# Optimization experiments

Measured on AMD Instinct MI355X. Metric: run time of the kernel, lower is better.

Reference implementation:

```python
import jax, jax.numpy as jnp
import numpy as np

B, S, D, H = 8, 1024, 1024, 16
DH = D // H
EPS = 1e-5


def _layernorm(x):
    # elementwise_affine=False LayerNorm, eps=1e-5
    m = jnp.mean(x, axis=-1, keepdims=True)
    v = jnp.var(x, axis=-1, keepdims=True)
    return (x - m) * jax.lax.rsqrt(v + EPS)


def setup_inputs() -> dict:
    key = jax.random.key(0)
    ks = jax.random.split(key, 11)
    s = 0.02
    return {
        "x": jax.random.normal(ks[0], (B, S, D), jnp.float32),
        "y": jax.random.normal(ks[1], (B, 1, D), jnp.float32),
        "w_adaln": jax.random.normal(ks[2], (6 * D, D), jnp.float32) * s,
        "b_adaln": jnp.zeros((6 * D,), jnp.float32),
        "w_qkv": jax.random.normal(ks[3], (3 * D, D), jnp.float32) * s,
        "w_proj": jax.random.normal(ks[4], (D, D), jnp.float32) * s,
        "b_proj": jnp.zeros((D,), jnp.float32),
        "w_fc1": jax.random.normal(ks[5], (4 * D, D), jnp.float32) * s,
        "b_fc1": jnp.zeros((4 * D,), jnp.float32),
        "w_fc2": jax.random.normal(ks[6], (D, 4 * D), jnp.float32) * s,
        "b_fc2": jnp.zeros((D,), jnp.float32),
    }


def reference(x, y, w_adaln, b_adaln, w_qkv, w_proj, b_proj, w_fc1, b_fc1, w_fc2, b_fc2):
    # adaLN-Zero modulation params from conditioning y: SiLU -> Linear -> 6 chunks
    mods = jax.nn.silu(y) @ w_adaln.T + b_adaln          # [B,1,6D]
    sh_a, sc_a, g_a, sh_m, sc_m, g_m = jnp.split(mods, 6, axis=-1)

    # --- attention branch ---
    xm = _layernorm(x) * (1.0 + sc_a) + sh_a             # modulate
    qkv = xm @ w_qkv.T                                   # [B,S,3D] (qkv_bias=False)
    q, k, v = [t.reshape(B, S, H, DH).transpose(0, 2, 1, 3) for t in jnp.split(qkv, 3, axis=-1)]
    scale = 1.0 / np.sqrt(DH)
    scores = jnp.einsum("bhqd,bhkd->bhqk", q, k) * scale  # unfused MATH-backend sdpa
    attn = jax.nn.softmax(scores, axis=-1)
    o = jnp.einsum("bhqk,bhkd->bhqd", attn, v)
    o = o.transpose(0, 2, 1, 3).reshape(B, S, D)
    o = o @ w_proj.T + b_proj
    x = x + g_a * o                                      # gated residual

    # --- MLP branch ---
    xm = _layernorm(x) * (1.0 + sc_m) + sh_m
    h = jax.nn.gelu(xm @ w_fc1.T + b_fc1, approximate=True)  # GELU(tanh)
    h = h @ w_fc2.T + b_fc2
    return x + g_m * h
```

## Files before the change

kernel.cpp:

```cpp
#include <hip/hip_runtime.h>

typedef __bf16 bf16;
typedef __attribute__((ext_vector_type(8))) __bf16 bf16x8;
typedef __attribute__((ext_vector_type(4))) __bf16 bf16x4;
typedef __attribute__((ext_vector_type(2))) __bf16 bf16x2;
typedef __attribute__((ext_vector_type(4))) float f32x4;

#define MFMA16(a, b, c) __builtin_amdgcn_mfma_f32_16x16x32_bf16((a), (b), (c), 0, 0, 0)

__device__ __forceinline__ float clampf(float v, float c) {
    return fminf(fmaxf(v, -c), c);
}

__device__ __forceinline__ void gload16(const void* g, void* l) {
    __builtin_amdgcn_global_load_lds((const __attribute__((address_space(1))) void*)g,
                                     (__attribute__((address_space(3))) void*)l, 16, 0, 0);
}

__launch_bounds__(256)
__global__ void cvt_kernel(const float* __restrict__ src, bf16* __restrict__ dst, int n4)
{
    int i = blockIdx.x * 256 + threadIdx.x;
    if (i < n4) {
        float4 v = ((const float4*)src)[i];
        bf16x4 o;
        o[0] = (bf16)v.x; o[1] = (bf16)v.y; o[2] = (bf16)v.z; o[3] = (bf16)v.w;
        ((bf16x4*)dst)[i] = o;
    }
}

__launch_bounds__(256)
__global__ void adaln_kernel(const float* __restrict__ y, const float* __restrict__ w,
                             const float* __restrict__ bias, float* __restrict__ mods)
{
    const int b = blockIdx.y;
    const int n = blockIdx.x * 256 + threadIdx.x;
    __shared__ float sy[1024];
    for (int i = threadIdx.x; i < 1024; i += 256) {
        float t = y[b * 1024 + i];
        sy[i] = t / (1.f + __expf(-t));
    }
    __syncthreads();
    const float* wr = w + (size_t)n * 1024;
    float acc = 0.f;
    for (int k = 0; k < 1024; k += 4) {
        float4 wv = *(const float4*)(wr + k);
        acc += sy[k] * wv.x + sy[k + 1] * wv.y + sy[k + 2] * wv.z + sy[k + 3] * wv.w;
    }
    mods[b * 6144 + n] = clampf(acc + bias[n], 64.f);
}

__launch_bounds__(256)
__global__ void ln_mod_kernel(const float* __restrict__ xin, const float* __restrict__ mods,
                              int shOff, int scOff, bf16* __restrict__ out)
{
    const int row = blockIdx.x;
    const int b = row >> 10;
    const int tid = threadIdx.x;
    const int wave = tid >> 6, lane = tid & 63;

    const float4 x4 = *((const float4*)xin + (size_t)row * 256 + tid);
    float v[4] = {x4.x, x4.y, x4.z, x4.w};

    float s = v[0] + v[1] + v[2] + v[3];
    float ss = v[0]*v[0] + v[1]*v[1] + v[2]*v[2] + v[3]*v[3];
#pragma unroll
    for (int o = 32; o > 0; o >>= 1) {
        s  += __shfl_xor(s, o, 64);
        ss += __shfl_xor(ss, o, 64);
    }
    __shared__ float red[8];
    if (lane == 0) { red[wave] = s; red[4 + wave] = ss; }
    __syncthreads();
    s  = red[0] + red[1] + red[2] + red[3];
    ss = red[4] + red[5] + red[6] + red[7];
    const float mean = s * (1.f / 1024.f);
    const float var  = ss * (1.f / 1024.f) - mean * mean;
    const float rstd = rsqrtf(fmaxf(var, 0.f) + 1e-5f);

    const float* mb = mods + b * 6144;
    bf16x4 o4;
#pragma unroll
    for (int j = 0; j < 4; ++j) {
        int c = tid * 4 + j;
        o4[j] = (bf16)clampf(((v[j] - mean) * rstd) * (1.f + mb[scOff + c]) + mb[shOff + c], 64.f);
    }
    *((bf16x4*)out + (size_t)row * 256 + tid) = o4;
}

template <int EPI>
__launch_bounds__(512, 2)
__global__ void gemm_8ph(const bf16* __restrict__ A, const bf16* __restrict__ W,
                         const float* __restrict__ bias, const float* __restrict__ mods,
                         int gateOff, const float* __restrict__ resid,
                         float* __restrict__ of, bf16* __restrict__ ob,
                         int N, int K, int nN, float clampV)
{
    __shared__ __align__(16) bf16 sm[2][2][2][8192];

    const int tid = threadIdx.x;
    const int wave = tid >> 6, lane = tid & 63, quad = lane >> 4, l16 = lane & 15;
    const int wm = wave >> 2, wn = wave & 3;

    const int cpx = gridDim.x >> 3;
    const int wg = ((int)blockIdx.x & 7) * cpx + ((int)blockIdx.x >> 3);
    const int tileM = (wg / nN) * 256;
    const int tileN = (wg % nN) * 256;

    const int p0 = tid * 16;
    const int l0 = p0 ^ (((p0 >> 7) & 7) << 4);
    const int srow = l0 >> 7;
    const int scol = (l0 & 127) >> 1;
    const bf16* Ag = A + (size_t)(tileM + srow) * K + scol;
    const bf16* Wg = W + (size_t)(tileN + srow) * K + scol;
    const size_t halfStep = (size_t)128 * K;
    const size_t slotStep = (size_t)64 * K;

    const int xorv = (l16 & 7) << 4;
    const int cx0 = (quad * 16) ^ xorv;
    const int cx1 = (64 + quad * 16) ^ xorv;
    const int bofs = (wn & 1) * 64;

    f32x4 acc[8][4] = {};
    bf16x8 af[4][2], b0[2][2], b1[2][2];

#define STAGE8(d, h, kt) do { \
        const bf16* g_ = ((h) < 2 ? Ag : Wg) + (size_t)((h) & 1) * halfStep + (size_t)(kt) * 64; \
        bf16* l_ = &sm[d][(h) >> 1][(h) & 1][wave * 512]; \
        gload16(g_, l_); \
        gload16(g_ + slotStep, l_ + 4096); \
    } while (0)

#define RD_AF8(d, mb) do { \
        _Pragma("unroll") for (int m_ = 0; m_ < 4; ++m_) { \
            const char* r_ = (const char*)&sm[d][0][wm][0] + ((mb) + m_ * 16 + l16) * 128; \
            af[m_][0] = *(const bf16x8*)(r_ + cx0); \
            af[m_][1] = *(const bf16x8*)(r_ + cx1); \
        } \
    } while (0)

#define RD_B8(d, arr, nb) do { \
        _Pragma("unroll") for (int n_ = 0; n_ < 2; ++n_) { \
            const char* r_ = (const char*)&sm[d][1][wn >> 1][0] + (bofs + (nb) + n_ * 16 + l16) * 128; \
            arr[n_][0] = *(const bf16x8*)(r_ + cx0); \
            arr[n_][1] = *(const bf16x8*)(r_ + cx1); \
        } \
    } while (0)

#define MM8(mb, arr, nb) do { \
        __builtin_amdgcn_s_setprio(1); \
        _Pragma("unroll") for (int m_ = 0; m_ < 4; ++m_) \
        _Pragma("unroll") for (int n_ = 0; n_ < 2; ++n_) { \
            acc[(mb) + m_][(nb) + n_] = MFMA16(af[m_][0], arr[n_][0], acc[(mb) + m_][(nb) + n_]); \
            acc[(mb) + m_][(nb) + n_] = MFMA16(af[m_][1], arr[n_][1], acc[(mb) + m_][(nb) + n_]); \
        } \
        __builtin_amdgcn_s_setprio(0); \
    } while (0)

#define BARF() do { __builtin_amdgcn_s_barrier(); asm volatile("" ::: "memory"); } while (0)
#define LGKM0() do { asm volatile("s_waitcnt lgkmcnt(0)" ::: "memory"); \
                     __builtin_amdgcn_sched_barrier(0); } while (0)
#define VMC2() do { asm volatile("s_waitcnt vmcnt(2)" ::: "memory"); \
                    __builtin_amdgcn_sched_barrier(0); } while (0)

    STAGE8(0, 0, 0); STAGE8(0, 1, 0); STAGE8(0, 2, 0); STAGE8(0, 3, 0);
    STAGE8(1, 0, 1);
    VMC2();
    BARF();

    const int nkt = K >> 6;
    for (int t = 0; t < nkt; t += 2) {
        const int t2 = (t + 2 < nkt) ? t + 2 : nkt - 1;
        const int t3 = (t + 3 < nkt) ? t + 3 : nkt - 1;
        RD_AF8(0, 0); RD_B8(0, b0, 0);
        STAGE8(1, 1, t + 1);
        BARF(); LGKM0();
        MM8(0, b0, 0);
        BARF();
        RD_B8(0, b1, 32);
        STAGE8(1, 2, t + 1);
        BARF(); LGKM0();
        MM8(0, b1, 2);
        BARF();
        RD_AF8(0, 64);
        STAGE8(1, 3, t + 1);
        BARF(); LGKM0();
        MM8(4, b1, 2);
        BARF();
        STAGE8(0, 0, t2);
        BARF();
        MM8(4, b0, 0);
        VMC2();
        BARF();
        RD_AF8(1, 0); RD_B8(1, b0, 0);
        STAGE8(0, 1, t2);
        BARF(); LGKM0();
        MM8(0, b0, 0);
        BARF();
        RD_B8(1, b1, 32);
        STAGE8(0, 2, t2);
        BARF(); LGKM0();
        MM8(0, b1, 2);
        BARF();
        RD_AF8(1, 64);
        STAGE8(0, 3, t2);
        BARF(); LGKM0();
        MM8(4, b1, 2);
        BARF();
        STAGE8(1, 0, t3);
        BARF();
        MM8(4, b0, 0);
        VMC2();
        BARF();
    }
    asm volatile("s_waitcnt vmcnt(0)" ::: "memory");

#undef STAGE8
#undef RD_AF8
#undef RD_B8
#undef MM8
#undef BARF
#undef LGKM0
#undef VMC2

    const int rowB = tileM + wm * 128 + quad * 4;
    const int colB = tileN + wn * 64 + l16;
#pragma unroll
    for (int mt = 0; mt < 8; ++mt) {
#pragma unroll
        for (int nt = 0; nt < 4; ++nt) {
            const int col = colB + nt * 16;
#pragma unroll
            for (int i = 0; i < 4; ++i) {
                const int row = rowB + mt * 16 + i;
                float v = acc[mt][nt][i];
                if (EPI != 0) v += bias[col];
                if (EPI == 0) {
                    ob[(size_t)row * N + col] = (bf16)clampf(v, clampV);
                } else if (EPI == 1) {
                    const int bb = row >> 10;
                    const float g = mods[bb * 6144 + gateOff + col];
                    of[(size_t)row * N + col] =
                        clampf(resid[(size_t)row * N + col] + g * v, clampV);
                } else {
                    const float e = __expf(1.5957691216f * (v + 0.044715f * v * v * v));
                    const float tt = 1.f - 2.f / (e + 1.f);
                    ob[(size_t)row * N + col] = (bf16)clampf(0.5f * v * (1.f + tt), clampV);
                }
            }
        }
    }
}

template <int EPI>
__launch_bounds__(256)
__global__ void gemm_bt(const bf16* __restrict__ A, const float* __restrict__ W,
                        const float* __restrict__ bias, const float* __restrict__ mods,
                        int gateOff, const float* __restrict__ resid,
                        float* __restrict__ of, bf16* __restrict__ ob,
                        int M, int N, int K, float clampV)
{
    constexpr int LDT = 40;
    __shared__ bf16 As[128 * LDT];
    __shared__ bf16 Bs[128 * LDT];

    const int tid = threadIdx.x;
    const int wave = tid >> 6, lane = tid & 63, quad = lane >> 4, l16 = lane & 15;
    const int wrow = wave >> 1, wcol = wave & 1;
    const int tileM = blockIdx.y * 128, tileN = blockIdx.x * 128;
    const int sr = tid >> 2;
    const int sk = (tid & 3) * 8;

    const bf16*  Ag = A + (size_t)(tileM + sr) * K + sk;
    const float* Wg = W + (size_t)(tileN + sr) * K + sk;

    f32x4 acc[4][4] = {};

    for (int k0 = 0; k0 < K; k0 += 32) {
        bf16x8 a0 = *(const bf16x8*)(Ag + k0);
        bf16x8 a1 = *(const bf16x8*)(Ag + (size_t)64 * K + k0);
        float4 w0a = *(const float4*)(Wg + k0);
        float4 w0b = *(const float4*)(Wg + k0 + 4);
        float4 w1a = *(const float4*)(Wg + (size_t)64 * K + k0);
        float4 w1b = *(const float4*)(Wg + (size_t)64 * K + k0 + 4);
        bf16x8 b0, b1;
        b0[0] = (bf16)w0a.x; b0[1] = (bf16)w0a.y; b0[2] = (bf16)w0a.z; b0[3] = (bf16)w0a.w;
        b0[4] = (bf16)w0b.x; b0[5] = (bf16)w0b.y; b0[6] = (bf16)w0b.z; b0[7] = (bf16)w0b.w;
        b1[0] = (bf16)w1a.x; b1[1] = (bf16)w1a.y; b1[2] = (bf16)w1a.z; b1[3] = (bf16)w1a.w;
        b1[4] = (bf16)w1b.x; b1[5] = (bf16)w1b.y; b1[6] = (bf16)w1b.z; b1[7] = (bf16)w1b.w;
        *(bf16x8*)&As[sr * LDT + sk] = a0;
        *(bf16x8*)&As[(sr + 64) * LDT + sk] = a1;
        *(bf16x8*)&Bs[sr * LDT + sk] = b0;
        *(bf16x8*)&Bs[(sr + 64) * LDT + sk] = b1;
        __syncthreads();

        bf16x8 af[4], bfr[4];
#pragma unroll
        for (int mt = 0; mt < 4; ++mt)
            af[mt] = *(const bf16x8*)&As[(wrow * 64 + mt * 16 + l16) * LDT + quad * 8];
#pragma unroll
        for (int nt = 0; nt < 4; ++nt)
            bfr[nt] = *(const bf16x8*)&Bs[(wcol * 64 + nt * 16 + l16) * LDT + quad * 8];
#pragma unroll
        for (int mt = 0; mt < 4; ++mt)
#pragma unroll
            for (int nt = 0; nt < 4; ++nt)
                acc[mt][nt] = MFMA16(af[mt], bfr[nt], acc[mt][nt]);
        __syncthreads();
    }

#pragma unroll
    for (int mt = 0; mt < 4; ++mt) {
#pragma unroll
        for (int nt = 0; nt < 4; ++nt) {
            const int col = tileN + wcol * 64 + nt * 16 + l16;
#pragma unroll
            for (int i = 0; i < 4; ++i) {
                const int row = tileM + wrow * 64 + mt * 16 + quad * 4 + i;
                float v = acc[mt][nt][i];
                if (EPI != 0) v += bias[col];
                if (EPI == 0) {
                    ob[(size_t)row * N + col] = (bf16)clampf(v, clampV);
                } else if (EPI == 1) {
                    const int bb = row >> 10;
                    const float g = mods[bb * 6144 + gateOff + col];
                    of[(size_t)row * N + col] =
                        clampf(resid[(size_t)row * N + col] + g * v, clampV);
                } else {
                    const float e = __expf(1.5957691216f * (v + 0.044715f * v * v * v));
                    const float t = 1.f - 2.f / (e + 1.f);
                    ob[(size_t)row * N + col] = (bf16)clampf(0.5f * v * (1.f + t), clampV);
                }
            }
        }
    }
}

__launch_bounds__(256)
__global__ void attn_kernel(const bf16* __restrict__ qkv, bf16* __restrict__ o)
{
    const int bid = blockIdx.x;
    const int qt = bid >> 7;
    const int b  = (bid >> 4) & 7;
    const int h  = bid & 15;
    const int tid = threadIdx.x;
    const int wave = tid >> 6, lane = tid & 63, quad = lane >> 4, l16 = lane & 15;

    __shared__ bf16 Kl[64 * 72];
    __shared__ bf16 Vt[64 * 72];
    __shared__ bf16 Pl[4][32 * 72];

    const size_t basebs = (size_t)b * 1024 * 3072;
    const int qbase = qt * 128 + wave * 32;

    bf16x8 qf[2][2];
#pragma unroll
    for (int mt = 0; mt < 2; ++mt)
#pragma unroll
        for (int kk = 0; kk < 2; ++kk) {
            const int row = qbase + mt * 16 + l16;
            const int dh = kk * 32 + quad * 8;
            qf[mt][kk] = *(const bf16x8*)(qkv + basebs + (size_t)row * 3072 + h * 64 + dh);
        }

    const int kr = tid >> 2, kc = (tid & 3) * 16;
    const int vp = tid >> 3, vc = (tid & 7) * 8;
    const bf16* Kg = qkv + basebs + (size_t)kr * 3072 + 1024 + h * 64 + kc;
    const bf16* Vg = qkv + basebs + (size_t)(2 * vp) * 3072 + 2048 + h * 64 + vc;
    const size_t ktStep = (size_t)64 * 3072;

    bf16x8 k0 = *(const bf16x8*)Kg;
    bf16x8 k1 = *(const bf16x8*)(Kg + 8);
    bf16x8 v0 = *(const bf16x8*)Vg;
    bf16x8 v1 = *(const bf16x8*)(Vg + 3072);

    f32x4 oacc[2][4] = {};
    float lsum[2][4] = {};

    for (int kt = 0; kt < 16; ++kt) {
        *(bf16x8*)&Kl[kr * 72 + kc] = k0;
        *(bf16x8*)&Kl[kr * 72 + kc + 8] = k1;
#pragma unroll
        for (int j = 0; j < 8; ++j) {
            bf16x2 pr; pr[0] = v0[j]; pr[1] = v1[j];
            *(bf16x2*)&Vt[(vc + j) * 72 + 2 * vp] = pr;
        }
        __syncthreads();

        const size_t noff = (size_t)(kt < 15 ? kt + 1 : 15) * ktStep;
        k0 = *(const bf16x8*)(Kg + noff);
        k1 = *(const bf16x8*)(Kg + noff + 8);
        v0 = *(const bf16x8*)(Vg + noff);
        v1 = *(const bf16x8*)(Vg + noff + 3072);

        f32x4 s[2][4] = {};
#pragma unroll
        for (int kk = 0; kk < 2; ++kk)
#pragma unroll
            for (int nt = 0; nt < 4; ++nt) {
                bf16x8 kf = *(const bf16x8*)&Kl[(nt * 16 + l16) * 72 + kk * 32 + quad * 8];
#pragma unroll
                for (int mt = 0; mt < 2; ++mt)
                    s[mt][nt] = MFMA16(qf[mt][kk], kf, s[mt][nt]);
            }

#pragma unroll
        for (int mt = 0; mt < 2; ++mt)
#pragma unroll
            for (int nt = 0; nt < 4; ++nt)
#pragma unroll
                for (int i = 0; i < 4; ++i) {
                    float p = exp2f(fminf(s[mt][nt][i] * 0.18033688f, 43.f));
                    Pl[wave][(mt * 16 + quad * 4 + i) * 72 + nt * 16 + l16] = (bf16)p;
                    lsum[mt][i] += p;
                }

#pragma unroll
        for (int kk = 0; kk < 2; ++kk) {
            bf16x8 pf[2];
#pragma unroll
            for (int mt = 0; mt < 2; ++mt)
                pf[mt] = *(const bf16x8*)&Pl[wave][(mt * 16 + l16) * 72 + kk * 32 + quad * 8];
#pragma unroll
            for (int nt = 0; nt < 4; ++nt) {
                bf16x8 vf = *(const bf16x8*)&Vt[(nt * 16 + l16) * 72 + kk * 32 + quad * 8];
#pragma unroll
                for (int mt = 0; mt < 2; ++mt)
                    oacc[mt][nt] = MFMA16(pf[mt], vf, oacc[mt][nt]);
            }
        }
        __syncthreads();
    }

    bf16* ob = o + (size_t)b * 1024 * 1024 + h * 64;
#pragma unroll
    for (int mt = 0; mt < 2; ++mt)
#pragma unroll
        for (int i = 0; i < 4; ++i) {
            float l = lsum[mt][i];
#pragma unroll
            for (int off = 1; off < 16; off <<= 1) l += __shfl_xor(l, off, 64);
            const float inv = 1.f / fmaxf(l, 1e-20f);
            const int row = qbase + mt * 16 + quad * 4 + i;
#pragma unroll
            for (int nt = 0; nt < 4; ++nt)
                ob[(size_t)row * 1024 + nt * 16 + l16] = (bf16)clampf(oacc[mt][nt][i] * inv, 16.f);
        }
}

extern "C" void kernel_launch(void* const* d_in, const int* in_sizes, int n_in,
                              void* d_out, int out_size, void* d_ws, size_t ws_size,
                              hipStream_t stream)
{
    const float* x       = (const float*)d_in[0];
    const float* y       = (const float*)d_in[1];
    const float* w_adaln = (const float*)d_in[2];
    const float* b_adaln = (const float*)d_in[3];
    const float* w_qkv   = (const float*)d_in[4];
    const float* w_proj  = (const float*)d_in[5];
    const float* b_proj  = (const float*)d_in[6];
    const float* w_fc1   = (const float*)d_in[7];
    const float* b_fc1   = (const float*)d_in[8];
    const float* w_fc2   = (const float*)d_in[9];
    const float* b_fc2   = (const float*)d_in[10];
    float* out = (float*)d_out;

    char* ws = (char*)d_ws;
    float* mods = (float*)ws;
    bf16* bufA  = (bf16*)(ws + (1ull << 18));
    bf16* bufH  = (bf16*)(ws + (1ull << 18) + (1ull << 24));
    size_t off = (1ull << 18) + (1ull << 24) + (1ull << 26);
    bf16* wb_qkv  = (bf16*)(ws + off);               off += 6ull << 20;
    bf16* wb_proj = (bf16*)(ws + off);               off += 2ull << 20;
    bf16* wb_fc1  = (bf16*)(ws + off);               off += 8ull << 20;
    bf16* wb_fc2  = (bf16*)(ws + off);               off += 8ull << 20;
    const bool fast = ws_size >= off;

    adaln_kernel<<<dim3(24, 8), 256, 0, stream>>>(y, w_adaln, b_adaln, mods);
    ln_mod_kernel<<<8192, 256, 0, stream>>>(x, mods, 0, 1024, bufA);

    if (fast) {
        cvt_kernel<<<(3072 * 256 + 255) / 256, 256, 0, stream>>>(w_qkv, wb_qkv, 3072 * 256);
        cvt_kernel<<<(1024 * 256 + 255) / 256, 256, 0, stream>>>(w_proj, wb_proj, 1024 * 256);
        cvt_kernel<<<(4096 * 256 + 255) / 256, 256, 0, stream>>>(w_fc1, wb_fc1, 4096 * 256);
        cvt_kernel<<<(4096 * 256 + 255) / 256, 256, 0, stream>>>(w_fc2, wb_fc2, 4096 * 256);

        gemm_8ph<0><<<32 * 12, 512, 0, stream>>>(bufA, wb_qkv, nullptr, nullptr, 0,
                                                 nullptr, nullptr, bufH, 3072, 1024, 12, 64.f);
        attn_kernel<<<1024, 256, 0, stream>>>(bufH, bufA);
        gemm_8ph<1><<<32 * 4, 512, 0, stream>>>(bufA, wb_proj, b_proj, mods, 2048,
                                                x, out, nullptr, 1024, 1024, 4, 64.f);
        ln_mod_kernel<<<8192, 256, 0, stream>>>(out, mods, 3072, 4096, bufA);
        gemm_8ph<2><<<32 * 16, 512, 0, stream>>>(bufA, wb_fc1, b_fc1, nullptr, 0,
                                                 nullptr, nullptr, bufH, 4096, 1024, 16, 64.f);
        gemm_8ph<1><<<32 * 4, 512, 0, stream>>>(bufH, wb_fc2, b_fc2, mods, 5120,
                                                out, out, nullptr, 1024, 4096, 4, 64.f);
    } else {
        gemm_bt<0><<<dim3(24, 64), 256, 0, stream>>>(bufA, w_qkv, nullptr, nullptr, 0,
                                                     nullptr, nullptr, bufH, 8192, 3072, 1024, 64.f);
        attn_kernel<<<1024, 256, 0, stream>>>(bufH, bufA);
        gemm_bt<1><<<dim3(8, 64), 256, 0, stream>>>(bufA, w_proj, b_proj, mods, 2048,
                                                    x, out, nullptr, 8192, 1024, 1024, 64.f);
        ln_mod_kernel<<<8192, 256, 0, stream>>>(out, mods, 3072, 4096, bufA);
        gemm_bt<2><<<dim3(32, 64), 256, 0, stream>>>(bufA, w_fc1, b_fc1, nullptr, 0,
                                                     nullptr, nullptr, bufH, 8192, 4096, 1024, 64.f);
        gemm_bt<1><<<dim3(8, 64), 256, 0, stream>>>(bufH, w_fc2, b_fc2, mods, 5120,
                                                    out, out, nullptr, 8192, 1024, 4096, 64.f);
    }
}
```

Baseline: 570.2 us.

## Add triple-buffered 256x128 GEMM kernel for QKV, proj and fc2

Adds a new bf16 GEMM kernel built on 256x128 tiles with a three-stage LDS ring filled by global_load_lds. K-tile loads are interleaved with half-tile MFMA phases, and the kernel uses XOR-swizzled LDS, an XCD-aware block remap, and launch bounds of two blocks per CU. It replaces the previous 8-phase kernel for the QKV, output-projection and fc2 GEMMs, which now run with more, smaller workgroups. The goal is better overlap of memory traffic with MFMA work and better occupancy on the narrow-N GEMMs, at the cost of a large LDS footprint and hand-tuned waitcnt ordering that could be fragile.

```diff
diff --git a/kernel.cpp b/kernel.cpp
--- a/kernel.cpp
+++ b/kernel.cpp
@@ -253,6 +253,137 @@
 }
 
 template <int EPI>
+__launch_bounds__(512, 2)
+__global__ void gemm_np(const bf16* __restrict__ A, const bf16* __restrict__ W,
+                        const float* __restrict__ bias, const float* __restrict__ mods,
+                        int gateOff, const float* __restrict__ resid,
+                        float* __restrict__ of, bf16* __restrict__ ob,
+                        int N, int K, int nN, float clampV)
+{
+    __shared__ __align__(16) bf16 sm[3][3][8192];
+
+    const int tid = threadIdx.x;
+    const int wave = tid >> 6, lane = tid & 63, quad = lane >> 4, l16 = lane & 15;
+    const int wm = wave >> 1, wn = wave & 1;
+
+    const int cpx = gridDim.x >> 3;
+    const int wg = ((int)blockIdx.x & 7) * cpx + ((int)blockIdx.x >> 3);
+    const int tileM = (wg / nN) * 256;
+    const int tileN = (wg % nN) * 128;
+
+    const int p0 = tid * 16;
+    const int l0 = p0 ^ (((p0 >> 7) & 7) << 4);
+    const int srow = l0 >> 7;
+    const int scol = (l0 & 127) >> 1;
+    const bf16* Ag  = A + (size_t)(tileM + srow) * K + scol;
+    const bf16* Ag2 = Ag + (size_t)128 * K;
+    const bf16* Wg  = W + (size_t)(tileN + srow) * K + scol;
+    const size_t slotStep = (size_t)64 * K;
+
+    const int xorv = (l16 & 7) << 4;
+    const int cx0 = (quad * 16) ^ xorv;
+    const int cx1 = (64 + quad * 16) ^ xorv;
+
+    f32x4 acc[4][4] = {};
+    bf16x8 af[4], bfr[4];
+
+#define SPASS(r2, reg, src, p, ts) \
+    gload16((src) + (size_t)(p) * slotStep + (size_t)(ts) * 64, \
+            &sm[r2][reg][(p) * 4096 + wave * 512])
+
+#define RDNP(r, cx) do { \
+        _Pragma("unroll") for (int q_ = 0; q_ < 4; ++q_) { \
+            af[q_]  = *(const bf16x8*)((const char*)&sm[r][wm >> 1][0] + \
+                        (((wm & 1) * 64 + q_ * 16 + l16) * 128) + (cx)); \
+            bfr[q_] = *(const bf16x8*)((const char*)&sm[r][2][0] + \
+                        ((wn * 64 + q_ * 16 + l16) * 128) + (cx)); \
+        } \
+    } while (0)
+
+#define MMNP() do { \
+        __builtin_amdgcn_s_setprio(1); \
+        _Pragma("unroll") for (int m_ = 0; m_ < 4; ++m_) \
+        _Pragma("unroll") for (int n_ = 0; n_ < 4; ++n_) \
+            acc[m_][n_] = MFMA16(af[m_], bfr[n_], acc[m_][n_]); \
+        __builtin_amdgcn_s_setprio(0); \
+    } while (0)
+
+#define BARF() do { __builtin_amdgcn_s_barrier(); asm volatile("" ::: "memory"); } while (0)
+#define LGKM0() do { asm volatile("s_waitcnt lgkmcnt(0)" ::: "memory"); \
+                     __builtin_amdgcn_sched_barrier(0); } while (0)
+#define VMC6() do { asm volatile("s_waitcnt vmcnt(6)" ::: "memory"); \
+                    __builtin_amdgcn_sched_barrier(0); } while (0)
+
+#define KTILE(r, r2, T) do { \
+        const int ts_ = ((T) + 2 < nkt) ? (T) + 2 : nkt - 1; \
+         \
+        RDNP(r, cx0); \
+        SPASS(r2, 0, Ag, 0, ts_); SPASS(r2, 0, Ag, 1, ts_); SPASS(r2, 1, Ag2, 0, ts_); \
+        BARF(); LGKM0(); \
+        MMNP(); \
+        BARF(); \
+         \
+        RDNP(r, cx1); \
+        SPASS(r2, 1, Ag2, 1, ts_); SPASS(r2, 2, Wg, 0, ts_); SPASS(r2, 2, Wg, 1, ts_); \
+        BARF(); LGKM0(); \
+        MMNP(); \
+        VMC6(); \
+        BARF(); \
+    } while (0)
+
+    const int nkt = K >> 6;
+    SPASS(0, 0, Ag, 0, 0); SPASS(0, 0, Ag, 1, 0); SPASS(0, 1, Ag2, 0, 0);
+    SPASS(0, 1, Ag2, 1, 0); SPASS(0, 2, Wg, 0, 0); SPASS(0, 2, Wg, 1, 0);
+    SPASS(1, 0, Ag, 0, 1); SPASS(1, 0, Ag, 1, 1); SPASS(1, 1, Ag2, 0, 1);
+    SPASS(1, 1, Ag2, 1, 1); SPASS(1, 2, Wg, 0, 1); SPASS(1, 2, Wg, 1, 1);
+    VMC6();
+    BARF();
+
+    for (int t = 0; t < nkt; t += 3) {
+        KTILE(0, 2, t);
+        if (t + 1 < nkt) KTILE(1, 0, t + 1);
+        if (t + 2 < nkt) KTILE(2, 1, t + 2);
+    }
+    asm volatile("s_waitcnt vmcnt(0)" ::: "memory");
+
+#undef SPASS
+#undef RDNP
+#undef MMNP
+#undef BARF
+#undef LGKM0
+#undef VMC6
+#undef KTILE
+
+    const int rowB = tileM + wm * 64 + quad * 4;
+    const int colB = tileN + wn * 64 + l16;
+#pragma unroll
+    for (int mt = 0; mt < 4; ++mt) {
+#pragma unroll
+        for (int nt = 0; nt < 4; ++nt) {
+            const int col = colB + nt * 16;
+#pragma unroll
+            for (int i = 0; i < 4; ++i) {
+                const int row = rowB + mt * 16 + i;
+                float v = acc[mt][nt][i];
+                if (EPI != 0) v += bias[col];
+                if (EPI == 0) {
+                    ob[(size_t)row * N + col] = (bf16)clampf(v, clampV);
+                } else if (EPI == 1) {
+                    const int bb = row >> 10;
+                    const float g = mods[bb * 6144 + gateOff + col];
+                    of[(size_t)row * N + col] =
+                        clampf(resid[(size_t)row * N + col] + g * v, clampV);
+                } else {
+                    const float e = __expf(1.5957691216f * (v + 0.044715f * v * v * v));
+                    const float tt = 1.f - 2.f / (e + 1.f);
+                    ob[(size_t)row * N + col] = (bf16)clampf(0.5f * v * (1.f + tt), clampV);
+                }
+            }
+        }
+    }
+}
+
+template <int EPI>
 __launch_bounds__(256)
 __global__ void gemm_bt(const bf16* __restrict__ A, const float* __restrict__ W,
                         const float* __restrict__ bias, const float* __restrict__ mods,
@@ -485,16 +616,16 @@
         cvt_kernel<<<(4096 * 256 + 255) / 256, 256, 0, stream>>>(w_fc1, wb_fc1, 4096 * 256);
         cvt_kernel<<<(4096 * 256 + 255) / 256, 256, 0, stream>>>(w_fc2, wb_fc2, 4096 * 256);
 
-        gemm_8ph<0><<<32 * 12, 512, 0, stream>>>(bufA, wb_qkv, nullptr, nullptr, 0,
-                                                 nullptr, nullptr, bufH, 3072, 1024, 12, 64.f);
+        gemm_np<0><<<768, 512, 0, stream>>>(bufA, wb_qkv, nullptr, nullptr, 0,
+                                            nullptr, nullptr, bufH, 3072, 1024, 24, 64.f);
         attn_kernel<<<1024, 256, 0, stream>>>(bufH, bufA);
-        gemm_8ph<1><<<32 * 4, 512, 0, stream>>>(bufA, wb_proj, b_proj, mods, 2048,
-                                                x, out, nullptr, 1024, 1024, 4, 64.f);
+        gemm_np<1><<<256, 512, 0, stream>>>(bufA, wb_proj, b_proj, mods, 2048,
+                                            x, out, nullptr, 1024, 1024, 8, 64.f);
         ln_mod_kernel<<<8192, 256, 0, stream>>>(out, mods, 3072, 4096, bufA);
         gemm_8ph<2><<<32 * 16, 512, 0, stream>>>(bufA, wb_fc1, b_fc1, nullptr, 0,
                                                  nullptr, nullptr, bufH, 4096, 1024, 16, 64.f);
-        gemm_8ph<1><<<32 * 4, 512, 0, stream>>>(bufH, wb_fc2, b_fc2, mods, 5120,
-                                                out, out, nullptr, 1024, 4096, 4, 64.f);
+        gemm_np<1><<<256, 512, 0, stream>>>(bufH, wb_fc2, b_fc2, mods, 5120,
+                                            out, out, nullptr, 1024, 4096, 8, 64.f);
     } else {
         gemm_bt<0><<<dim3(24, 64), 256, 0, stream>>>(bufA, w_qkv, nullptr, nullptr, 0,
                                                      nullptr, nullptr, bufH, 8192, 3072, 1024, 64.f);
```

Result: faster. 523.4 us (-8.2%).
